# Kernel optimization log

Hardware: AMD Instinct MI355X
Metric: run time of the kernel (lower is better)

## Reference

```python
import jax, jax.numpy as jnp
import numpy as np

EPS = 1.1920929e-07  # torch RMSNorm default eps = finfo(float32).eps

def rmsnorm(x, w):
    return x * jax.lax.rsqrt(jnp.mean(x * x, axis=-1, keepdims=True) + EPS) * w

def setup_inputs() -> dict:
    key = jax.random.key(0)
    ks = jax.random.split(key, 12)
    D, H, SC, ST = 1024, 16, 64, 16
    B, T = 2, 2048
    s = 0.02
    return {
        "x": jax.random.normal(ks[0], (B, T, D), jnp.float32),
        "qkv_w": jax.random.normal(ks[1], (3 * D, D), jnp.float32) * s,
        "o_w": jax.random.normal(ks[2], (D, D), jnp.float32) * s,
        "norm1_w": jnp.ones((D,), jnp.float32),
        "norm2_w": jnp.ones((D,), jnp.float32),
        "in_w": jax.random.normal(ks[3], (SC, D), jnp.float32) * s,
        "out_w": jax.random.normal(ks[4], (D, SC), jnp.float32) * s,  # zeros in torch init; randn for nontrivial baseline
        "A_log": jax.random.normal(ks[5], (SC, ST), jnp.float32) * 0.1,
        "Bp_w": jax.random.normal(ks[6], (ST, SC), jnp.float32) * s,
        "Cp_w": jax.random.normal(ks[7], (ST, SC), jnp.float32) * s,
        "dt_w": jax.random.normal(ks[8], (SC, SC), jnp.float32) * s,
        "dt_b": jnp.full((SC,), -3.0, jnp.float32),
        "gate_w": jax.random.normal(ks[9], (SC, D), jnp.float32) * s,
    }

def selective_scan(h, in_w, out_w, A_log, Bp_w, Cp_w, dt_w, dt_b, gate_w):
    B, T, D = h.shape
    SC, ST = A_log.shape
    z = h @ in_w.T                      # [B,T,SC]
    gate = jax.nn.silu(h @ gate_w.T)    # [B,T,SC]
    A = -jnp.exp(A_log)                 # [SC,ST]
    Bi = z @ Bp_w.T                     # [B,T,ST]
    Ci = z @ Cp_w.T                     # [B,T,ST]
    dt = jax.nn.softplus(z @ dt_w.T + dt_b)  # [B,T,SC]
    A_bar = 1.0 + dt[..., None] * A     # [B,T,SC,ST]

    def step(state, inp):
        a_bar, dtz_t, b_t, c_t = inp    # [B,SC,ST],[B,SC],[B,ST],[B,ST]
        state = a_bar * state + dtz_t[:, :, None] * b_t[:, None, :]
        y = jnp.sum(state * c_t[:, None, :], axis=-1)  # [B,SC]
        return state, y

    init = jnp.zeros((B, SC, ST), h.dtype)
    xs = (jnp.swapaxes(A_bar, 0, 1), jnp.swapaxes(dt * z, 0, 1),
          jnp.swapaxes(Bi, 0, 1), jnp.swapaxes(Ci, 0, 1))
    _, ys = jax.lax.scan(step, init, xs)      # [T,B,SC]
    y = jnp.swapaxes(ys, 0, 1) * gate         # [B,T,SC]
    return y @ out_w.T                        # [B,T,D]

def reference(x, qkv_w, o_w, norm1_w, norm2_w, in_w, out_w, A_log, Bp_w, Cp_w, dt_w, dt_b, gate_w):
    B, T, D = x.shape
    H = 16
    hd = D // H
    h = rmsnorm(x, norm1_w)
    qkv = (h @ qkv_w.T).reshape(B, T, 3, H, hd)
    qkv = jnp.transpose(qkv, (2, 0, 3, 1, 4))  # [3,B,H,T,hd]
    q, k, v = qkv[0], qkv[1], qkv[2]
    attn = jnp.einsum('bhqd,bhkd->bhqk', q, k) / np.sqrt(hd).astype(np.float32)
    mask = jnp.tril(jnp.ones((T, T), bool))
    attn = jnp.where(mask, attn, -jnp.inf)
    attn = jax.nn.softmax(attn, axis=-1)
    out = jnp.einsum('bhqk,bhkd->bhqd', attn, v)
    out = jnp.transpose(out, (0, 2, 1, 3)).reshape(B, T, D)
    x = x + out @ o_w.T
    h2 = rmsnorm(x, norm2_w)
    x = x + selective_scan(h2, in_w, out_w, A_log, Bp_w, Cp_w, dt_w, dt_b, gate_w)
    return x
```

## Files before the change

kernel.cpp:

```cpp
#include <hip/hip_runtime.h>
#include <hip/hip_bf16.h>
#include <math.h>

typedef __hip_bfloat16 bf16;
typedef __attribute__((ext_vector_type(4))) float v_f32x4;
typedef __attribute__((ext_vector_type(4))) unsigned short v_u16x4;
typedef __attribute__((ext_vector_type(8))) unsigned short v_u16x8;
typedef __attribute__((ext_vector_type(8))) __bf16 v_bf16x8;

#define NB 2
#define NT 2048
#define ND 1024
#define NH 16
#define NSC 64
#define NST 16
#define NM (NB*NT)
#define RMS_EPS 1.1920929e-07f
#define NCHUNK 32
#define CLEN 64

__device__ inline float b2f(unsigned short u) {
  union { unsigned int i; float f; } v; v.i = ((unsigned int)u) << 16; return v.f;
}
__device__ inline unsigned short f2b(float f) {
  union { float f; unsigned int i; } v; v.f = f;
  unsigned int r = (v.i + 0x7FFF + ((v.i >> 16) & 1)) >> 16;
  return (unsigned short)r;
}

__device__ inline void gl_lds16(const bf16* g, bf16* l) {
  __builtin_amdgcn_global_load_lds((__attribute__((address_space(1))) void*)g,
                                   (__attribute__((address_space(3))) void*)l,
                                   16, 0, 0);
}

__global__ __launch_bounds__(256) void cvt_kernel(const float* __restrict__ src,
                                                  bf16* __restrict__ dst, int n4) {
  int i = blockIdx.x * 256 + threadIdx.x;
  if (i < n4) {
    v_f32x4 v = ((const v_f32x4*)src)[i];
    v_u16x4 o;
    o[0] = f2b(v[0]); o[1] = f2b(v[1]); o[2] = f2b(v[2]); o[3] = f2b(v[3]);
    ((v_u16x4*)dst)[i] = o;
  }
}

__global__ __launch_bounds__(256) void rmsnorm_kernel(
    const float* __restrict__ x, const float* __restrict__ w, bf16* __restrict__ out) {
  const int row = blockIdx.x;
  const int t = threadIdx.x;
  v_f32x4 xv = *(const v_f32x4*)(x + (size_t)row * ND + t * 4);
  float s = xv[0]*xv[0] + xv[1]*xv[1] + xv[2]*xv[2] + xv[3]*xv[3];
  #pragma unroll
  for (int off = 32; off; off >>= 1) s += __shfl_xor(s, off, 64);
  __shared__ float red[4];
  __shared__ float scale_s;
  if ((t & 63) == 0) red[t >> 6] = s;
  __syncthreads();
  if (t == 0) {
    float tot = red[0] + red[1] + red[2] + red[3];
    scale_s = rsqrtf(tot * (1.0f / ND) + RMS_EPS);
  }
  __syncthreads();
  float sc = scale_s;
  v_f32x4 wv = *(const v_f32x4*)(w + t * 4);
  unsigned short* orow = (unsigned short*)out + (size_t)row * ND + t * 4;
  v_u16x4 o;
  o[0] = f2b(xv[0] * sc * wv[0]);
  o[1] = f2b(xv[1] * sc * wv[1]);
  o[2] = f2b(xv[2] * sc * wv[2]);
  o[3] = f2b(xv[3] * sc * wv[3]);
  *(v_u16x4*)orow = o;
}

template <bool RES, bool OUTF32>
__global__ __launch_bounds__(256) void gemm_bt_kernel(
    const bf16* __restrict__ A, const bf16* __restrict__ Bw,
    const float* __restrict__ res, void* __restrict__ Cout, int N, int K, int lda) {
  __shared__ alignas(16) bf16 As[128 * 32];
  __shared__ alignas(16) bf16 Bs[128 * 32];
  const int tid = threadIdx.x;
  const int wid = tid >> 6;
  const int lane = tid & 63;
  const int c = lane & 15;
  const int quad = lane >> 4;
  const int m0 = blockIdx.y * 128;
  const int n0 = blockIdx.x * 128;
  const int wm = (wid >> 1) * 64;
  const int wn = (wid & 1) * 64;
  const int srow = tid >> 2;
  const int schunk = tid & 3;

  const bf16* Ap0 = A + (size_t)(m0 + srow) * lda + schunk * 8;
  const bf16* Ap1 = Ap0 + (size_t)64 * lda;
  const bf16* Bp0 = Bw + (size_t)(n0 + srow) * K + schunk * 8;
  const bf16* Bp1 = Bp0 + (size_t)64 * K;
  bf16* AsW0 = As + wid * 512;
  bf16* AsW1 = As + 2048 + wid * 512;
  bf16* BsW0 = Bs + wid * 512;
  bf16* BsW1 = Bs + 2048 + wid * 512;

  v_f32x4 acc[4][4];
  #pragma unroll
  for (int i = 0; i < 4; i++)
    #pragma unroll
    for (int j = 0; j < 4; j++)
      #pragma unroll
      for (int r = 0; r < 4; r++) acc[i][j][r] = 0.0f;

  const int nk = K >> 5;
  for (int kt = 0; kt < nk; kt++) {
    gl_lds16(Ap0 + kt * 32, AsW0);
    gl_lds16(Ap1 + kt * 32, AsW1);
    gl_lds16(Bp0 + kt * 32, BsW0);
    gl_lds16(Bp1 + kt * 32, BsW1);
    __syncthreads();
    v_bf16x8 af[4], bfw[4];
    #pragma unroll
    for (int i = 0; i < 4; i++)
      af[i] = *(const v_bf16x8*)&As[(wm + i * 16 + c) * 32 + quad * 8];
    #pragma unroll
    for (int j = 0; j < 4; j++)
      bfw[j] = *(const v_bf16x8*)&Bs[(wn + j * 16 + c) * 32 + quad * 8];
    #pragma unroll
    for (int i = 0; i < 4; i++)
      #pragma unroll
      for (int j = 0; j < 4; j++)
        acc[i][j] = __builtin_amdgcn_mfma_f32_16x16x32_bf16(af[i], bfw[j], acc[i][j], 0, 0, 0);
    __syncthreads();
  }

  #pragma unroll
  for (int i = 0; i < 4; i++)
    #pragma unroll
    for (int j = 0; j < 4; j++)
      #pragma unroll
      for (int r = 0; r < 4; r++) {
        int rg = m0 + wm + i * 16 + quad * 4 + r;
        int cg = n0 + wn + j * 16 + c;
        size_t idx = (size_t)rg * N + cg;
        float v = acc[i][j][r];
        if (RES) v += res[idx];
        if (OUTF32) ((float*)Cout)[idx] = v;
        else ((bf16*)Cout)[idx] = __float2bfloat16(v);
      }
}

template <bool OUTF32>
__global__ __launch_bounds__(256) void gemm_skinny_kernel(
    const bf16* __restrict__ A, const bf16* __restrict__ Bw,
    void* __restrict__ Cout, int K, int lda) {
  __shared__ alignas(16) bf16 As[16 * 32];
  __shared__ alignas(16) bf16 Bs[128 * 32];
  const int tid = threadIdx.x;
  const int w = tid >> 6;
  const int lane = tid & 63;
  const int c = lane & 15;
  const int quad = lane >> 4;
  const int m0 = blockIdx.x * 16;
  const int lrow = lane >> 2, lchunk = lane & 3;

  const bf16* ApL = A + (size_t)(m0 + lrow) * lda + lchunk * 8;
  const bf16* BpL0 = Bw + (size_t)(w * 16 + lrow) * K + lchunk * 8;
  const bf16* BpL1 = Bw + (size_t)(64 + w * 16 + lrow) * K + lchunk * 8;
  bf16* BsW0 = Bs + w * 512;
  bf16* BsW1 = Bs + 2048 + w * 512;

  v_f32x4 acc[2];
  #pragma unroll
  for (int j = 0; j < 2; j++)
    #pragma unroll
    for (int r = 0; r < 4; r++) acc[j][r] = 0.0f;

  const int nk = K >> 5;
  for (int kt = 0; kt < nk; kt++) {
    if (w == 0) gl_lds16(ApL + kt * 32, As);
    gl_lds16(BpL0 + kt * 32, BsW0);
    gl_lds16(BpL1 + kt * 32, BsW1);
    __syncthreads();
    v_bf16x8 af = *(const v_bf16x8*)&As[c * 32 + quad * 8];
    #pragma unroll
    for (int j = 0; j < 2; j++) {
      v_bf16x8 bfw = *(const v_bf16x8*)&Bs[(w * 32 + j * 16 + c) * 32 + quad * 8];
      acc[j] = __builtin_amdgcn_mfma_f32_16x16x32_bf16(af, bfw, acc[j], 0, 0, 0);
    }
    __syncthreads();
  }

  #pragma unroll
  for (int j = 0; j < 2; j++)
    #pragma unroll
    for (int r = 0; r < 4; r++) {
      size_t idx = (size_t)(m0 + quad * 4 + r) * 128 + w * 32 + j * 16 + c;
      if (OUTF32) ((float*)Cout)[idx] = acc[j][r];
      else ((bf16*)Cout)[idx] = __float2bfloat16(acc[j][r]);
    }
}

__global__ __launch_bounds__(256) void vtrans_kernel(const bf16* __restrict__ qkv,
                                                     bf16* __restrict__ VtG) {
  __shared__ alignas(16) bf16 Vs[64 * 72];
  const int tid = threadIdx.x;
  const int t0 = blockIdx.x * 64;
  const int bh = blockIdx.y;
  const int b = bh >> 4, h = bh & 15;
  const int srow = tid >> 2, schunk = tid & 3;
  {
    const bf16* src = qkv + (size_t)(b * NT + t0 + srow) * 3072 + 2048 + h * 64 + schunk * 16;
    *(v_u16x8*)&Vs[srow * 72 + schunk * 16] = *(const v_u16x8*)src;
    *(v_u16x8*)&Vs[srow * 72 + schunk * 16 + 8] = *(const v_u16x8*)(src + 8);
  }
  __syncthreads();
  const unsigned short* Vsu = (const unsigned short*)Vs;
  v_u16x8 a, bvec;
  #pragma unroll
  for (int i = 0; i < 8; i++) a[i] = Vsu[(schunk * 16 + i) * 72 + srow];
  #pragma unroll
  for (int i = 0; i < 8; i++) bvec[i] = Vsu[(schunk * 16 + 8 + i) * 72 + srow];
  bf16* dst = VtG + (size_t)(bh * 64 + srow) * NT + t0 + schunk * 16;
  *(v_u16x8*)dst = a;
  *(v_u16x8*)(dst + 8) = bvec;
}

__global__ __launch_bounds__(256) void attn_kernel(const bf16* __restrict__ qkv,
                                                   const bf16* __restrict__ VtG,
                                                   bf16* __restrict__ out) {
  __shared__ alignas(16) bf16 Qs[64 * 72];
  __shared__ alignas(16) bf16 Ks[64 * 72];
  __shared__ alignas(16) bf16 Vt[64 * 72];
  __shared__ alignas(16) bf16 Ps[64 * 72];
  const int tid = threadIdx.x;
  const int w = tid >> 6;
  const int lane = tid & 63;
  const int c = lane & 15;
  const int quad = lane >> 4;
  const int id = blockIdx.x;
  const int bh = id & 31;
  const int j5 = id >> 5;
  const int j0 = j5 & 7;
  const int qt = (j5 & 24) | (((j5 >> 3) & 1) ? (7 - j0) : j0);
  const int b = bh >> 4;
  const int h = bh & 15;
  const int srow = tid >> 2;
  const int schunk = tid & 3;

  {
    const bf16* src = qkv + (size_t)(b * NT + qt * 64 + srow) * 3072 + h * 64 + schunk * 16;
    *(v_u16x8*)&Qs[srow * 72 + schunk * 16] = *(const v_u16x8*)src;
    *(v_u16x8*)&Qs[srow * 72 + schunk * 16 + 8] = *(const v_u16x8*)(src + 8);
  }
  __syncthreads();
  v_bf16x8 aq0 = *(const v_bf16x8*)&Qs[(w * 16 + c) * 72 + quad * 8];
  v_bf16x8 aq1 = *(const v_bf16x8*)&Qs[(w * 16 + c) * 72 + 32 + quad * 8];

  float l_part[4];
  v_f32x4 o[4];
  #pragma unroll
  for (int r = 0; r < 4; r++) l_part[r] = 0.0f;
  #pragma unroll
  for (int j = 0; j < 4; j++)
    #pragma unroll
    for (int r = 0; r < 4; r++) o[j][r] = 0.0f;

  for (int kt = 0; kt <= qt; kt++) {
    {
      const bf16* ksrc = qkv + (size_t)(b * NT + kt * 64 + srow) * 3072 + 1024 + h * 64 + schunk * 16;
      *(v_u16x8*)&Ks[srow * 72 + schunk * 16] = *(const v_u16x8*)ksrc;
      *(v_u16x8*)&Ks[srow * 72 + schunk * 16 + 8] = *(const v_u16x8*)(ksrc + 8);
      const bf16* vsrc = VtG + (size_t)(bh * 64 + srow) * NT + kt * 64 + schunk * 16;
      *(v_u16x8*)&Vt[srow * 72 + schunk * 16] = *(const v_u16x8*)vsrc;
      *(v_u16x8*)&Vt[srow * 72 + schunk * 16 + 8] = *(const v_u16x8*)(vsrc + 8);
    }
    __syncthreads();

    const bool diag = (kt == qt);
    #pragma unroll
    for (int j = 0; j < 4; j++) {
      v_bf16x8 bk0 = *(const v_bf16x8*)&Ks[(j * 16 + c) * 72 + quad * 8];
      v_bf16x8 bk1 = *(const v_bf16x8*)&Ks[(j * 16 + c) * 72 + 32 + quad * 8];
      v_f32x4 z;
      #pragma unroll
      for (int r = 0; r < 4; r++) z[r] = 0.0f;
      z = __builtin_amdgcn_mfma_f32_16x16x32_bf16(aq0, bk0, z, 0, 0, 0);
      z = __builtin_amdgcn_mfma_f32_16x16x32_bf16(aq1, bk1, z, 0, 0, 0);
      #pragma unroll
      for (int r = 0; r < 4; r++) {
        float s = fminf(z[r] * 0.125f, 60.0f);
        float p = __expf(s);
        if (diag && (j * 16 + c) > (w * 16 + quad * 4 + r)) p = 0.0f;
        l_part[r] += p;
        Ps[(w * 16 + quad * 4 + r) * 72 + j * 16 + c] = __float2bfloat16(p);
      }
    }
    #pragma unroll
    for (int ks = 0; ks < 2; ks++) {
      v_bf16x8 ap = *(const v_bf16x8*)&Ps[(w * 16 + c) * 72 + ks * 32 + quad * 8];
      #pragma unroll
      for (int jn = 0; jn < 4; jn++) {
        v_bf16x8 bv = *(const v_bf16x8*)&Vt[(jn * 16 + c) * 72 + ks * 32 + quad * 8];
        o[jn] = __builtin_amdgcn_mfma_f32_16x16x32_bf16(ap, bv, o[jn], 0, 0, 0);
      }
    }
    __syncthreads();
  }

  #pragma unroll
  for (int r = 0; r < 4; r++) {
    float l = l_part[r];
    l += __shfl_xor(l, 1, 64);
    l += __shfl_xor(l, 2, 64);
    l += __shfl_xor(l, 4, 64);
    l += __shfl_xor(l, 8, 64);
    l_part[r] = l;
  }

  #pragma unroll
  for (int jn = 0; jn < 4; jn++)
    #pragma unroll
    for (int r = 0; r < 4; r++) {
      int qg = qt * 64 + w * 16 + quad * 4 + r;
      out[(size_t)(b * NT + qg) * ND + h * 64 + jn * 16 + c] =
          __float2bfloat16(o[jn][r] / l_part[r]);
    }
}

__global__ __launch_bounds__(256) void scanprep_kernel(
    const bf16* __restrict__ zg, const float* __restrict__ P2, const float* __restrict__ dt_b,
    float* __restrict__ dt_a, float* __restrict__ dtz_a, float* __restrict__ gate_a) {
  const int row = blockIdx.x * 4 + (threadIdx.x >> 6);
  const int c = threadIdx.x & 63;
  const unsigned short* zgu = (const unsigned short*)zg;
  float z = b2f(zgu[(size_t)row * 128 + c]);
  float g = b2f(zgu[(size_t)row * 128 + 64 + c]);
  float a = P2[(size_t)row * 128 + c] + dt_b[c];
  float dt = (a > 20.0f) ? a : log1pf(__expf(a));
  dt_a[(size_t)row * NSC + c] = dt;
  dtz_a[(size_t)row * NSC + c] = dt * z;
  gate_a[(size_t)row * NSC + c] = g / (1.0f + __expf(-g));
}

__global__ __launch_bounds__(256) void scanA_kernel(
    const float* __restrict__ dt_a, const float* __restrict__ dtz_a,
    const float* __restrict__ P2, const float* __restrict__ A_log,
    float* __restrict__ Pbuf, float* __restrict__ Sbuf) {
  __shared__ float dtS[CLEN * 16], dtzS[CLEN * 16], biS[CLEN * 16];
  const int k = blockIdx.x, scg = blockIdx.y, b = blockIdx.z;
  const int tid = threadIdx.x;
  const int t0 = k * CLEN;
  {
    int r = tid >> 2, c4 = (tid & 3) * 4;
    *(v_f32x4*)&dtS[r * 16 + c4]  = *(const v_f32x4*)&dt_a[(size_t)(b * NT + t0 + r) * NSC + scg * 16 + c4];
    *(v_f32x4*)&dtzS[r * 16 + c4] = *(const v_f32x4*)&dtz_a[(size_t)(b * NT + t0 + r) * NSC + scg * 16 + c4];
    *(v_f32x4*)&biS[r * 16 + c4]  = *(const v_f32x4*)&P2[(size_t)(b * NT + t0 + r) * 128 + 64 + c4];
  }
  __syncthreads();
  const int st = tid & 15, scl = tid >> 4;
  const float A = -__expf(A_log[(scg * 16 + scl) * NST + st]);
  float P = 1.0f, s = 0.0f;
  #pragma unroll
  for (int t = 0; t < CLEN; t++) {
    float a = fmaf(dtS[t * 16 + scl], A, 1.0f);
    float u = dtzS[t * 16 + scl] * biS[t * 16 + st];
    P *= a;
    s = fmaf(a, s, u);
  }
  size_t idx = (size_t)(b * NCHUNK + k) * 1024 + scg * 256 + tid;
  Pbuf[idx] = P;
  Sbuf[idx] = s;
}

__global__ __launch_bounds__(1024) void scanB_kernel(
    const float* __restrict__ Pbuf, const float* __restrict__ Sbuf,
    float* __restrict__ init) {
  const int b = blockIdx.x;
  const int tid = threadIdx.x;
  float P[NCHUNK], S[NCHUNK];
  #pragma unroll
  for (int kk = 0; kk < NCHUNK; kk++) {
    size_t idx = (size_t)(b * NCHUNK + kk) * 1024 + tid;
    P[kk] = Pbuf[idx];
    S[kk] = Sbuf[idx];
  }
  float s = 0.0f;
  #pragma unroll
  for (int kk = 0; kk < NCHUNK; kk++) {
    init[(size_t)(b * NCHUNK + kk) * 1024 + tid] = s;
    s = fmaf(P[kk], s, S[kk]);
  }
}

__global__ __launch_bounds__(256) void scanC_kernel(
    const float* __restrict__ dt_a, const float* __restrict__ dtz_a,
    const float* __restrict__ P2, const float* __restrict__ gate_a,
    const float* __restrict__ A_log, const float* __restrict__ init,
    bf16* __restrict__ ys) {
  __shared__ float dtS[CLEN * 16], dtzS[CLEN * 16], biS[CLEN * 16], ciS[CLEN * 16], gS[CLEN * 16];
  const int k = blockIdx.x, scg = blockIdx.y, b = blockIdx.z;
  const int tid = threadIdx.x;
  const int t0 = k * CLEN;
  {
    int r = tid >> 2, c4 = (tid & 3) * 4;
    *(v_f32x4*)&dtS[r * 16 + c4]  = *(const v_f32x4*)&dt_a[(size_t)(b * NT + t0 + r) * NSC + scg * 16 + c4];
    *(v_f32x4*)&dtzS[r * 16 + c4] = *(const v_f32x4*)&dtz_a[(size_t)(b * NT + t0 + r) * NSC + scg * 16 + c4];
    *(v_f32x4*)&biS[r * 16 + c4]  = *(const v_f32x4*)&P2[(size_t)(b * NT + t0 + r) * 128 + 64 + c4];
    *(v_f32x4*)&ciS[r * 16 + c4]  = *(const v_f32x4*)&P2[(size_t)(b * NT + t0 + r) * 128 + 80 + c4];
    *(v_f32x4*)&gS[r * 16 + c4]   = *(const v_f32x4*)&gate_a[(size_t)(b * NT + t0 + r) * NSC + scg * 16 + c4];
  }
  __syncthreads();
  const int st = tid & 15, scl = tid >> 4;
  const float A = -__expf(A_log[(scg * 16 + scl) * NST + st]);
  float s = init[(size_t)(b * NCHUNK + k) * 1024 + scg * 256 + tid];
  for (int t = 0; t < CLEN; t++) {
    float a = fmaf(dtS[t * 16 + scl], A, 1.0f);
    float u = dtzS[t * 16 + scl] * biS[t * 16 + st];
    s = fmaf(a, s, u);
    float pv = s * ciS[t * 16 + st];
    pv += __shfl_xor(pv, 1, 64);
    pv += __shfl_xor(pv, 2, 64);
    pv += __shfl_xor(pv, 4, 64);
    pv += __shfl_xor(pv, 8, 64);
    if (st == 0)
      ys[(size_t)(b * NT + t0 + t) * NSC + scg * 16 + scl] = __float2bfloat16(pv * gS[t * 16 + scl]);
  }
}

extern "C" void kernel_launch(void* const* d_in, const int* in_sizes, int n_in,
                              void* d_out, int out_size, void* d_ws, size_t ws_size,
                              hipStream_t stream) {
  const float* x      = (const float*)d_in[0];
  const float* qkv_w  = (const float*)d_in[1];
  const float* o_w    = (const float*)d_in[2];
  const float* n1w    = (const float*)d_in[3];
  const float* n2w    = (const float*)d_in[4];
  const float* in_w   = (const float*)d_in[5];
  const float* out_w  = (const float*)d_in[6];
  const float* A_log  = (const float*)d_in[7];
  const float* Bp_w   = (const float*)d_in[8];
  const float* Cp_w   = (const float*)d_in[9];
  const float* dt_w   = (const float*)d_in[10];
  const float* dt_b   = (const float*)d_in[11];
  const float* gate_w = (const float*)d_in[12];
  float* out = (float*)d_out;

  char* ws = (char*)d_ws;
  size_t off = 0;
  auto alloc = [&](size_t bytes) {
    char* p = ws + off;
    off += (bytes + 255) & ~(size_t)255;
    return p;
  };
  bf16* qkvw_b = (bf16*)alloc((size_t)3 * ND * ND * 2);
  bf16* ow_b   = (bf16*)alloc((size_t)ND * ND * 2);
  bf16* outw_b = (bf16*)alloc((size_t)ND * NSC * 2);
  bf16* W1     = (bf16*)alloc((size_t)128 * ND * 2);
  bf16* W2     = (bf16*)alloc((size_t)128 * NSC * 2);
  char* region0 = alloc((size_t)NM * 3 * ND * 2);
  char* region1 = alloc((size_t)NM * ND * 2);
  bf16* VtG    = (bf16*)alloc((size_t)NB * NH * 64 * NT * 2);
  bf16*  zg    = (bf16*)alloc((size_t)NM * 128 * 2);
  float* P2    = (float*)alloc((size_t)NM * 128 * 4);
  float* dt_a  = (float*)alloc((size_t)NM * NSC * 4);
  float* dtz_a = (float*)alloc((size_t)NM * NSC * 4);
  float* gate_a= (float*)alloc((size_t)NM * NSC * 4);
  bf16*  ys    = (bf16*)alloc((size_t)NM * NSC * 2);
  float* Pbuf  = (float*)alloc((size_t)NB * NCHUNK * 1024 * 4);
  float* Sbuf  = (float*)alloc((size_t)NB * NCHUNK * 1024 * 4);
  float* initb = (float*)alloc((size_t)NB * NCHUNK * 1024 * 4);

  bf16*  qkv     = (bf16*)region0;
  float* x1      = (float*)region0;
  bf16*  h       = (bf16*)region1;
  bf16*  attnout = (bf16*)region1;
  bf16*  h2      = (bf16*)region1;

  hipMemsetAsync(W2, 0, (size_t)128 * NSC * 2, stream);
  auto cvt = [&](const float* s, bf16* d, int n) {
    int n4 = n >> 2;
    cvt_kernel<<<(n4 + 255) / 256, 256, 0, stream>>>(s, d, n4);
  };
  cvt(qkv_w, qkvw_b, 3 * ND * ND);
  cvt(o_w, ow_b, ND * ND);
  cvt(out_w, outw_b, ND * NSC);
  cvt(in_w, W1, NSC * ND);
  cvt(gate_w, W1 + (size_t)NSC * ND, NSC * ND);
  cvt(dt_w, W2, NSC * NSC);
  cvt(Bp_w, W2 + NSC * NSC, NST * NSC);
  cvt(Cp_w, W2 + NSC * NSC + NST * NSC, NST * NSC);

  rmsnorm_kernel<<<NM, 256, 0, stream>>>(x, n1w, h);
  gemm_bt_kernel<false, false><<<dim3(3 * ND / 128, NM / 128), 256, 0, stream>>>(
      h, qkvw_b, nullptr, (void*)qkv, 3 * ND, ND, ND);
  vtrans_kernel<<<dim3(NT / 64, NB * NH), 256, 0, stream>>>(qkv, VtG);
  attn_kernel<<<(NT / 64) * NB * NH, 256, 0, stream>>>(qkv, VtG, attnout);
  gemm_bt_kernel<true, true><<<dim3(ND / 128, NM / 128), 256, 0, stream>>>(
      attnout, ow_b, x, (void*)x1, ND, ND, ND);
  rmsnorm_kernel<<<NM, 256, 0, stream>>>(x1, n2w, h2);
  gemm_skinny_kernel<false><<<NM / 16, 256, 0, stream>>>(h2, W1, (void*)zg, ND, ND);
  gemm_skinny_kernel<true><<<NM / 16, 256, 0, stream>>>(zg, W2, (void*)P2, NSC, 128);
  scanprep_kernel<<<NM / 4, 256, 0, stream>>>(zg, P2, dt_b, dt_a, dtz_a, gate_a);
  scanA_kernel<<<dim3(NCHUNK, 4, NB), 256, 0, stream>>>(dt_a, dtz_a, P2, A_log, Pbuf, Sbuf);
  scanB_kernel<<<NB, 1024, 0, stream>>>(Pbuf, Sbuf, initb);
  scanC_kernel<<<dim3(NCHUNK, 4, NB), 256, 0, stream>>>(dt_a, dtz_a, P2, gate_a, A_log, initb, ys);
  gemm_bt_kernel<true, true><<<dim3(ND / 128, NM / 128), 256, 0, stream>>>(
      ys, outw_b, x1, (void*)out, ND, NSC, NSC);
}
```

Measured before the change: 299.5 us.

## Merge weight conversions, widen attention query tile, add 64-row GEMM for small-N outputs

Merges the eight weight-conversion launches and the memset into one dispatch kernel. Attention now gives each block 128 query rows that share one K/V tile load, which halves K/V traffic and balances causal work by pairing tiles. A 64x128-tile GEMM replaces the 128x128 one for the o_proj and out_proj GEMMs, doubling the block count for better CU fill. It also drops the clamp on the exponent before exp, which risks overflow if scores are ever large, and the larger LDS footprint may lower occupancy.

```diff
diff --git a/kernel.cpp b/kernel.cpp
--- a/kernel.cpp
+++ b/kernel.cpp
@@ -34,15 +34,35 @@
                                    16, 0, 0);
 }
 
-__global__ __launch_bounds__(256) void cvt_kernel(const float* __restrict__ src,
-                                                  bf16* __restrict__ dst, int n4) {
-  int i = blockIdx.x * 256 + threadIdx.x;
-  if (i < n4) {
-    v_f32x4 v = ((const v_f32x4*)src)[i];
-    v_u16x4 o;
-    o[0] = f2b(v[0]); o[1] = f2b(v[1]); o[2] = f2b(v[2]); o[3] = f2b(v[3]);
-    ((v_u16x4*)dst)[i] = o;
-  }
+__global__ __launch_bounds__(256) void cvt_all_kernel(
+    const float* __restrict__ qkv_w, const float* __restrict__ o_w,
+    const float* __restrict__ out_w, const float* __restrict__ in_w,
+    const float* __restrict__ gate_w, const float* __restrict__ dt_w,
+    const float* __restrict__ Bp_w, const float* __restrict__ Cp_w,
+    bf16* __restrict__ qkvw_b, bf16* __restrict__ ow_b, bf16* __restrict__ outw_b,
+    bf16* __restrict__ W1, bf16* __restrict__ W2) {
+  const int blk = blockIdx.x, t = threadIdx.x;
+  const float* src; bf16* dst; int base;
+  if (blk < 3072)      { src = qkv_w;  dst = qkvw_b;      base = blk; }
+  else if (blk < 4096) { src = o_w;    dst = ow_b;        base = blk - 3072; }
+  else if (blk < 4160) { src = out_w;  dst = outw_b;      base = blk - 4096; }
+  else if (blk < 4224) { src = in_w;   dst = W1;          base = blk - 4160; }
+  else if (blk < 4288) { src = gate_w; dst = W1 + 65536;  base = blk - 4224; }
+  else if (blk < 4292) { src = dt_w;   dst = W2;          base = blk - 4288; }
+  else if (blk == 4292){ src = Bp_w;   dst = W2 + 4096;   base = 0; }
+  else if (blk == 4293){ src = Cp_w;   dst = W2 + 5120;   base = 0; }
+  else {
+    v_u16x8 z;
+    #pragma unroll
+    for (int i = 0; i < 8; i++) z[i] = 0;
+    *(v_u16x8*)(W2 + 6144 + t * 8) = z;
+    return;
+  }
+  int i = base * 256 + t;
+  v_f32x4 v = ((const v_f32x4*)src)[i];
+  v_u16x4 o;
+  o[0] = f2b(v[0]); o[1] = f2b(v[1]); o[2] = f2b(v[2]); o[3] = f2b(v[3]);
+  ((v_u16x4*)dst)[i] = o;
 }
 
 __global__ __launch_bounds__(256) void rmsnorm_kernel(
@@ -146,6 +166,76 @@
       }
 }
 
+template <bool RES, bool OUTF32>
+__global__ __launch_bounds__(256) void gemm_bt64_kernel(
+    const bf16* __restrict__ A, const bf16* __restrict__ Bw,
+    const float* __restrict__ res, void* __restrict__ Cout, int N, int K, int lda) {
+  __shared__ alignas(16) bf16 As[64 * 32];
+  __shared__ alignas(16) bf16 Bs[128 * 32];
+  const int tid = threadIdx.x;
+  const int wid = tid >> 6;
+  const int lane = tid & 63;
+  const int c = lane & 15;
+  const int quad = lane >> 4;
+  const int m0 = blockIdx.y * 64;
+  const int n0 = blockIdx.x * 128;
+  const int wm = (wid & 1) * 32;
+  const int wn = (wid >> 1) * 64;
+  const int srow = tid >> 2;
+  const int schunk = tid & 3;
+
+  const bf16* Ap = A + (size_t)(m0 + srow) * lda + schunk * 8;
+  const bf16* Bp0 = Bw + (size_t)(n0 + srow) * K + schunk * 8;
+  const bf16* Bp1 = Bp0 + (size_t)64 * K;
+  bf16* AsW  = As + wid * 512;
+  bf16* BsW0 = Bs + wid * 512;
+  bf16* BsW1 = Bs + 2048 + wid * 512;
+
+  v_f32x4 acc[2][4];
+  #pragma unroll
+  for (int i = 0; i < 2; i++)
+    #pragma unroll
+    for (int j = 0; j < 4; j++)
+      #pragma unroll
+      for (int r = 0; r < 4; r++) acc[i][j][r] = 0.0f;
+
+  const int nk = K >> 5;
+  for (int kt = 0; kt < nk; kt++) {
+    gl_lds16(Ap + kt * 32, AsW);
+    gl_lds16(Bp0 + kt * 32, BsW0);
+    gl_lds16(Bp1 + kt * 32, BsW1);
+    __syncthreads();
+    v_bf16x8 af[2], bfw[4];
+    #pragma unroll
+    for (int i = 0; i < 2; i++)
+      af[i] = *(const v_bf16x8*)&As[(wm + i * 16 + c) * 32 + quad * 8];
+    #pragma unroll
+    for (int j = 0; j < 4; j++)
+      bfw[j] = *(const v_bf16x8*)&Bs[(wn + j * 16 + c) * 32 + quad * 8];
+    #pragma unroll
+    for (int i = 0; i < 2; i++)
+      #pragma unroll
+      for (int j = 0; j < 4; j++)
+        acc[i][j] = __builtin_amdgcn_mfma_f32_16x16x32_bf16(af[i], bfw[j], acc[i][j], 0, 0, 0);
+    __syncthreads();
+  }
+
+  #pragma unroll
+  for (int i = 0; i < 2; i++)
+    #pragma unroll
+    for (int j = 0; j < 4; j++)
+      #pragma unroll
+      for (int r = 0; r < 4; r++) {
+        int rg = m0 + wm + i * 16 + quad * 4 + r;
+        int cg = n0 + wn + j * 16 + c;
+        size_t idx = (size_t)rg * N + cg;
+        float v = acc[i][j][r];
+        if (RES) v += res[idx];
+        if (OUTF32) ((float*)Cout)[idx] = v;
+        else ((bf16*)Cout)[idx] = __float2bfloat16(v);
+      }
+}
+
 template <bool OUTF32>
 __global__ __launch_bounds__(256) void gemm_skinny_kernel(
     const bf16* __restrict__ A, const bf16* __restrict__ Bw,
@@ -225,10 +315,10 @@
 __global__ __launch_bounds__(256) void attn_kernel(const bf16* __restrict__ qkv,
                                                    const bf16* __restrict__ VtG,
                                                    bf16* __restrict__ out) {
-  __shared__ alignas(16) bf16 Qs[64 * 72];
+  __shared__ alignas(16) bf16 Qs[128 * 72];
   __shared__ alignas(16) bf16 Ks[64 * 72];
   __shared__ alignas(16) bf16 Vt[64 * 72];
-  __shared__ alignas(16) bf16 Ps[64 * 72];
+  __shared__ alignas(16) bf16 Ps[128 * 72];
   const int tid = threadIdx.x;
   const int w = tid >> 6;
   const int lane = tid & 63;
@@ -237,32 +327,42 @@
   const int id = blockIdx.x;
   const int bh = id & 31;
   const int j5 = id >> 5;
-  const int j0 = j5 & 7;
-  const int qt = (j5 & 24) | (((j5 >> 3) & 1) ? (7 - j0) : j0);
+  const int qt2 = (j5 & 8) ? (15 - (j5 & 7)) : (j5 & 7);
   const int b = bh >> 4;
   const int h = bh & 15;
   const int srow = tid >> 2;
   const int schunk = tid & 3;
-
-  {
-    const bf16* src = qkv + (size_t)(b * NT + qt * 64 + srow) * 3072 + h * 64 + schunk * 16;
-    *(v_u16x8*)&Qs[srow * 72 + schunk * 16] = *(const v_u16x8*)src;
-    *(v_u16x8*)&Qs[srow * 72 + schunk * 16 + 8] = *(const v_u16x8*)(src + 8);
+  const int qbase = qt2 * 128;
+
+  #pragma unroll
+  for (int g = 0; g < 2; g++) {
+    const bf16* src = qkv + (size_t)(b * NT + qbase + g * 64 + srow) * 3072 + h * 64 + schunk * 16;
+    *(v_u16x8*)&Qs[(g * 64 + srow) * 72 + schunk * 16] = *(const v_u16x8*)src;
+    *(v_u16x8*)&Qs[(g * 64 + srow) * 72 + schunk * 16 + 8] = *(const v_u16x8*)(src + 8);
   }
   __syncthreads();
-  v_bf16x8 aq0 = *(const v_bf16x8*)&Qs[(w * 16 + c) * 72 + quad * 8];
-  v_bf16x8 aq1 = *(const v_bf16x8*)&Qs[(w * 16 + c) * 72 + 32 + quad * 8];
-
-  float l_part[4];
-  v_f32x4 o[4];
-  #pragma unroll
-  for (int r = 0; r < 4; r++) l_part[r] = 0.0f;
-  #pragma unroll
-  for (int j = 0; j < 4; j++)
-    #pragma unroll
-    for (int r = 0; r < 4; r++) o[j][r] = 0.0f;
-
-  for (int kt = 0; kt <= qt; kt++) {
+  v_bf16x8 aq[2][2];
+  #pragma unroll
+  for (int g = 0; g < 2; g++) {
+    aq[g][0] = *(const v_bf16x8*)&Qs[(g * 64 + w * 16 + c) * 72 + quad * 8];
+    aq[g][1] = *(const v_bf16x8*)&Qs[(g * 64 + w * 16 + c) * 72 + 32 + quad * 8];
+  }
+
+  float l_part[2][4];
+  v_f32x4 o[2][4];
+  #pragma unroll
+  for (int g = 0; g < 2; g++)
+    #pragma unroll
+    for (int r = 0; r < 4; r++) l_part[g][r] = 0.0f;
+  #pragma unroll
+  for (int g = 0; g < 2; g++)
+    #pragma unroll
+    for (int j = 0; j < 4; j++)
+      #pragma unroll
+      for (int r = 0; r < 4; r++) o[g][j][r] = 0.0f;
+
+  const int ktmax = 2 * qt2 + 1;
+  for (int kt = 0; kt <= ktmax; kt++) {
     {
       const bf16* ksrc = qkv + (size_t)(b * NT + kt * 64 + srow) * 3072 + 1024 + h * 64 + schunk * 16;
       *(v_u16x8*)&Ks[srow * 72 + schunk * 16] = *(const v_u16x8*)ksrc;
@@ -273,55 +373,64 @@
     }
     __syncthreads();
 
-    const bool diag = (kt == qt);
-    #pragma unroll
-    for (int j = 0; j < 4; j++) {
-      v_bf16x8 bk0 = *(const v_bf16x8*)&Ks[(j * 16 + c) * 72 + quad * 8];
-      v_bf16x8 bk1 = *(const v_bf16x8*)&Ks[(j * 16 + c) * 72 + 32 + quad * 8];
-      v_f32x4 z;
-      #pragma unroll
-      for (int r = 0; r < 4; r++) z[r] = 0.0f;
-      z = __builtin_amdgcn_mfma_f32_16x16x32_bf16(aq0, bk0, z, 0, 0, 0);
-      z = __builtin_amdgcn_mfma_f32_16x16x32_bf16(aq1, bk1, z, 0, 0, 0);
-      #pragma unroll
-      for (int r = 0; r < 4; r++) {
-        float s = fminf(z[r] * 0.125f, 60.0f);
-        float p = __expf(s);
-        if (diag && (j * 16 + c) > (w * 16 + quad * 4 + r)) p = 0.0f;
-        l_part[r] += p;
-        Ps[(w * 16 + quad * 4 + r) * 72 + j * 16 + c] = __float2bfloat16(p);
+    #pragma unroll
+    for (int g = 0; g < 2; g++) {
+      const int ktd = 2 * qt2 + g;
+      if (kt <= ktd) {
+        const bool diag = (kt == ktd);
+        #pragma unroll
+        for (int j4 = 0; j4 < 4; j4++) {
+          v_bf16x8 bk0 = *(const v_bf16x8*)&Ks[(j4 * 16 + c) * 72 + quad * 8];
+          v_bf16x8 bk1 = *(const v_bf16x8*)&Ks[(j4 * 16 + c) * 72 + 32 + quad * 8];
+          v_f32x4 z;
+          #pragma unroll
+          for (int r = 0; r < 4; r++) z[r] = 0.0f;
+          z = __builtin_amdgcn_mfma_f32_16x16x32_bf16(aq[g][0], bk0, z, 0, 0, 0);
+          z = __builtin_amdgcn_mfma_f32_16x16x32_bf16(aq[g][1], bk1, z, 0, 0, 0);
+          #pragma unroll
+          for (int r = 0; r < 4; r++) {
+            float p = __expf(z[r] * 0.125f);
+            if (diag && (j4 * 16 + c) > (w * 16 + quad * 4 + r)) p = 0.0f;
+            l_part[g][r] += p;
+            Ps[(g * 64 + w * 16 + quad * 4 + r) * 72 + j4 * 16 + c] = __float2bfloat16(p);
+          }
+        }
+        #pragma unroll
+        for (int ks = 0; ks < 2; ks++) {
+          v_bf16x8 ap = *(const v_bf16x8*)&Ps[(g * 64 + w * 16 + c) * 72 + ks * 32 + quad * 8];
+          #pragma unroll
+          for (int jn = 0; jn < 4; jn++) {
+            v_bf16x8 bv = *(const v_bf16x8*)&Vt[(jn * 16 + c) * 72 + ks * 32 + quad * 8];
+            o[g][jn] = __builtin_amdgcn_mfma_f32_16x16x32_bf16(ap, bv, o[g][jn], 0, 0, 0);
+          }
+        }
       }
     }
-    #pragma unroll
-    for (int ks = 0; ks < 2; ks++) {
-      v_bf16x8 ap = *(const v_bf16x8*)&Ps[(w * 16 + c) * 72 + ks * 32 + quad * 8];
-      #pragma unroll
-      for (int jn = 0; jn < 4; jn++) {
-        v_bf16x8 bv = *(const v_bf16x8*)&Vt[(jn * 16 + c) * 72 + ks * 32 + quad * 8];
-        o[jn] = __builtin_amdgcn_mfma_f32_16x16x32_bf16(ap, bv, o[jn], 0, 0, 0);
+    __syncthreads();
+  }
+
+  #pragma unroll
+  for (int g = 0; g < 2; g++)
+    #pragma unroll
+    for (int r = 0; r < 4; r++) {
+      float l = l_part[g][r];
+      l += __shfl_xor(l, 1, 64);
+      l += __shfl_xor(l, 2, 64);
+      l += __shfl_xor(l, 4, 64);
+      l += __shfl_xor(l, 8, 64);
+      l_part[g][r] = l;
+    }
+
+  #pragma unroll
+  for (int g = 0; g < 2; g++)
+    #pragma unroll
+    for (int jn = 0; jn < 4; jn++)
+      #pragma unroll
+      for (int r = 0; r < 4; r++) {
+        int qg = qbase + g * 64 + w * 16 + quad * 4 + r;
+        out[(size_t)(b * NT + qg) * ND + h * 64 + jn * 16 + c] =
+            __float2bfloat16(o[g][jn][r] / l_part[g][r]);
       }
-    }
-    __syncthreads();
-  }
-
-  #pragma unroll
-  for (int r = 0; r < 4; r++) {
-    float l = l_part[r];
-    l += __shfl_xor(l, 1, 64);
-    l += __shfl_xor(l, 2, 64);
-    l += __shfl_xor(l, 4, 64);
-    l += __shfl_xor(l, 8, 64);
-    l_part[r] = l;
-  }
-
-  #pragma unroll
-  for (int jn = 0; jn < 4; jn++)
-    #pragma unroll
-    for (int r = 0; r < 4; r++) {
-      int qg = qt * 64 + w * 16 + quad * 4 + r;
-      out[(size_t)(b * NT + qg) * ND + h * 64 + jn * 16 + c] =
-          __float2bfloat16(o[jn][r] / l_part[r]);
-    }
 }
 
 __global__ __launch_bounds__(256) void scanprep_kernel(
@@ -473,26 +582,14 @@
   bf16*  attnout = (bf16*)region1;
   bf16*  h2      = (bf16*)region1;
 
-  hipMemsetAsync(W2, 0, (size_t)128 * NSC * 2, stream);
-  auto cvt = [&](const float* s, bf16* d, int n) {
-    int n4 = n >> 2;
-    cvt_kernel<<<(n4 + 255) / 256, 256, 0, stream>>>(s, d, n4);
-  };
-  cvt(qkv_w, qkvw_b, 3 * ND * ND);
-  cvt(o_w, ow_b, ND * ND);
-  cvt(out_w, outw_b, ND * NSC);
-  cvt(in_w, W1, NSC * ND);
-  cvt(gate_w, W1 + (size_t)NSC * ND, NSC * ND);
-  cvt(dt_w, W2, NSC * NSC);
-  cvt(Bp_w, W2 + NSC * NSC, NST * NSC);
-  cvt(Cp_w, W2 + NSC * NSC + NST * NSC, NST * NSC);
-
+  cvt_all_kernel<<<4295, 256, 0, stream>>>(qkv_w, o_w, out_w, in_w, gate_w, dt_w,
+                                           Bp_w, Cp_w, qkvw_b, ow_b, outw_b, W1, W2);
   rmsnorm_kernel<<<NM, 256, 0, stream>>>(x, n1w, h);
   gemm_bt_kernel<false, false><<<dim3(3 * ND / 128, NM / 128), 256, 0, stream>>>(
       h, qkvw_b, nullptr, (void*)qkv, 3 * ND, ND, ND);
   vtrans_kernel<<<dim3(NT / 64, NB * NH), 256, 0, stream>>>(qkv, VtG);
-  attn_kernel<<<(NT / 64) * NB * NH, 256, 0, stream>>>(qkv, VtG, attnout);
-  gemm_bt_kernel<true, true><<<dim3(ND / 128, NM / 128), 256, 0, stream>>>(
+  attn_kernel<<<(NT / 128) * NB * NH, 256, 0, stream>>>(qkv, VtG, attnout);
+  gemm_bt64_kernel<true, true><<<dim3(ND / 128, NM / 64), 256, 0, stream>>>(
       attnout, ow_b, x, (void*)x1, ND, ND, ND);
   rmsnorm_kernel<<<NM, 256, 0, stream>>>(x1, n2w, h2);
   gemm_skinny_kernel<false><<<NM / 16, 256, 0, stream>>>(h2, W1, (void*)zg, ND, ND);
@@ -501,6 +598,6 @@
   scanA_kernel<<<dim3(NCHUNK, 4, NB), 256, 0, stream>>>(dt_a, dtz_a, P2, A_log, Pbuf, Sbuf);
   scanB_kernel<<<NB, 1024, 0, stream>>>(Pbuf, Sbuf, initb);
   scanC_kernel<<<dim3(NCHUNK, 4, NB), 256, 0, stream>>>(dt_a, dtz_a, P2, gate_a, A_log, initb, ys);
-  gemm_bt_kernel<true, true><<<dim3(ND / 128, NM / 128), 256, 0, stream>>>(
+  gemm_bt64_kernel<true, true><<<dim3(ND / 128, NM / 64), 256, 0, stream>>>(
       ys, outw_b, x1, (void*)out, ND, NSC, NSC);
 }
```

Measured after the change: 300.3 us. Within noise of the previous version (+0.3%).
